# Kernel optimization log

Hardware: AMD Instinct MI355X
Metric: run time of the kernel (lower is better)

Reference implementation:

```python
import jax, jax.numpy as jnp
import numpy as np

B, T, C, H = 2, 2048, 1024, 16
D = C // H  # head_dim = 64

def setup_inputs() -> dict:
    key = jax.random.key(0)
    k1, k2, k3, k4, k5 = jax.random.split(key, 5)
    x = jax.random.normal(k1, (B, T, C), dtype=jnp.float32)
    # RoPE tables (realistic frequencies)
    inv_freq = 1.0 / (10000.0 ** (jnp.arange(0, D // 2, dtype=jnp.float32) / (D // 2)))
    pos = jnp.arange(T, dtype=jnp.float32)
    ang = pos[:, None] * inv_freq[None, :]          # (T, D/2)
    cos, sin = jnp.cos(ang), jnp.sin(ang)
    # causal mask (True = keep)
    mask = jnp.tril(jnp.ones((T, T), dtype=bool))
    W_qkv = jax.random.normal(k2, (3 * C, C), dtype=jnp.float32) * (1.0 / np.sqrt(C))
    W_out = jax.random.normal(k3, (C, C), dtype=jnp.float32) * (1.0 / np.sqrt(C))
    return {"x": x, "cos": cos, "sin": sin, "mask": mask, "W_qkv": W_qkv, "W_out": W_out}

def apply_rope(x, cos, sin):
    # x: (B, H, T, D); cos/sin: (T, D/2)
    d = x.shape[-1] // 2
    x1, x2 = x[..., :d], x[..., d:]
    c = cos[None, None, :x.shape[2], :]
    s = sin[None, None, :x.shape[2], :]
    return jnp.concatenate([x1 * c - x2 * s, x2 * c + x1 * s], axis=-1)

def reference(x, cos, sin, mask, W_qkv, W_out):
    b, t, c = x.shape
    qkv = (x @ W_qkv.T).reshape(b, t, 3, H, D)
    q, k, v = qkv[:, :, 0], qkv[:, :, 1], qkv[:, :, 2]   # (b, t, H, D)
    q = q.transpose(0, 2, 1, 3)
    k = k.transpose(0, 2, 1, 3)
    v = v.transpose(0, 2, 1, 3)                           # (b, H, t, D)
    q = apply_rope(q, cos, sin)
    k = apply_rope(k, cos, sin)
    attn = jnp.einsum('bhqd,bhkd->bhqk', q, k) / jnp.sqrt(jnp.asarray(D, x.dtype))
    attn = jnp.where(mask[None, None, :, :], attn, -jnp.inf)
    attn = jax.nn.softmax(attn, axis=-1)
    out = jnp.einsum('bhqk,bhkd->bhqd', attn, v)          # (b, H, t, D)
    out = out.transpose(0, 2, 1, 3).reshape(b, t, c)
    return out @ W_out.T
```

## Files before the change

### kernel.cpp

```cpp
#include <hip/hip_runtime.h>
#include <stdint.h>

typedef __bf16 bf16;
typedef __bf16 bf16x4 __attribute__((ext_vector_type(4)));
typedef __bf16 bf16x8 __attribute__((ext_vector_type(8)));
typedef float f32x4 __attribute__((ext_vector_type(4)));

#define TSEQ 2048
#define NHEAD 16
#define HDIM 64
#define CDIM 1024

#define AS1(p) ((const __attribute__((address_space(1))) void*)(p))
#define AS3(p) ((__attribute__((address_space(3))) void*)(p))

#if __has_builtin(__builtin_amdgcn_exp2f)
#define EXP2(x) __builtin_amdgcn_exp2f(x)
#else
#define EXP2(x) exp2f(x)
#endif

__global__ __launch_bounds__(256) void cast3_bf16(const float* __restrict__ in1, int n1,
                                                  const float* __restrict__ in2, int n2,
                                                  const float* __restrict__ in3, int n3,
                                                  bf16* __restrict__ out1,
                                                  bf16* __restrict__ out2,
                                                  bf16* __restrict__ out3) {
  int i = (blockIdx.x * 256 + threadIdx.x) * 8;
  const float* src;
  bf16* dst;
  if (i < n1) {
    src = in1 + i; dst = out1 + i;
  } else if (i < n1 + n2) {
    src = in2 + (i - n1); dst = out2 + (i - n1);
  } else if (i < n1 + n2 + n3) {
    src = in3 + (i - n1 - n2); dst = out3 + (i - n1 - n2);
  } else {
    return;
  }
  float4 a = *(const float4*)src;
  float4 b = *(const float4*)(src + 4);
  bf16x8 r;
  r[0] = (bf16)a.x; r[1] = (bf16)a.y; r[2] = (bf16)a.z; r[3] = (bf16)a.w;
  r[4] = (bf16)b.x; r[5] = (bf16)b.y; r[6] = (bf16)b.z; r[7] = (bf16)b.w;
  *(bf16x8*)dst = r;
}

__global__ __launch_bounds__(256) void gemm_qkv_rope(const bf16* __restrict__ A,
                                                     const bf16* __restrict__ B,
                                                     const float* __restrict__ cosb,
                                                     const float* __restrict__ sinb,
                                                     bf16* __restrict__ Qb,
                                                     bf16* __restrict__ Kb,
                                                     bf16* __restrict__ Vt) {
  constexpr int K = 1024;
  __shared__ bf16 smem[8704];
  const int t = threadIdx.x;
  const int w = t >> 6, l = t & 63, g = l >> 4, ln = l & 15;
  const int wm = (w >> 1) * 64, wn = (w & 1) * 64;
  const int m0 = blockIdx.x * 128, n0 = blockIdx.y * 128;
  const int r0 = t >> 2, kc0 = (t & 3) * 8;

  f32x4 acc[4][4] = {};

  for (int k0 = 0; k0 < K; k0 += 32) {
    __syncthreads();
    __builtin_amdgcn_global_load_lds(AS1(A + (size_t)(m0 + r0) * K + k0 + kc0),
                                     AS3(&smem[t * 8]), 16, 0, 0);
    __builtin_amdgcn_global_load_lds(AS1(A + (size_t)(m0 + r0 + 64) * K + k0 + kc0),
                                     AS3(&smem[(t + 256) * 8]), 16, 0, 0);
    __builtin_amdgcn_global_load_lds(AS1(B + (size_t)(n0 + r0) * K + k0 + kc0),
                                     AS3(&smem[4096 + t * 8]), 16, 0, 0);
    __builtin_amdgcn_global_load_lds(AS1(B + (size_t)(n0 + r0 + 64) * K + k0 + kc0),
                                     AS3(&smem[4096 + (t + 256) * 8]), 16, 0, 0);
    __syncthreads();
    bf16x8 af[4], bfr[4];
#pragma unroll
    for (int i = 0; i < 4; i++) {
      af[i] = *(const bf16x8*)&smem[(wm + i * 16 + ln) * 32 + g * 8];
      bfr[i] = *(const bf16x8*)&smem[4096 + (wn + i * 16 + ln) * 32 + g * 8];
    }
#pragma unroll
    for (int i = 0; i < 4; i++)
#pragma unroll
      for (int j = 0; j < 4; j++)
        acc[i][j] = __builtin_amdgcn_mfma_f32_16x16x32_bf16(af[i], bfr[j], acc[i][j], 0, 0, 0);
  }

  const int part = n0 >> 10;
  if (part < 2) {
    bf16* dst = part ? Kb : Qb;
    const float qs = part ? 1.0f : 0.18033688011112042f;
#pragma unroll
    for (int i = 0; i < 4; i++)
#pragma unroll
      for (int j = 0; j < 2; j++) {
        int nl = (n0 & 1023) + wn + j * 16 + ln;
        int h = nl >> 6, d = nl & 31;
#pragma unroll
        for (int r = 0; r < 4; r++) {
          int row = m0 + wm + i * 16 + g * 4 + r;
          int tok = row & (TSEQ - 1), bb = row >> 11;
          float c = cosb[tok * 32 + d], s = sinb[tok * 32 + d];
          float a1 = acc[i][j][r], a2 = acc[i][j + 2][r];
          size_t ob = ((size_t)(bb * NHEAD + h) * TSEQ + tok) * HDIM + d;
          dst[ob] = (bf16)((a1 * c - a2 * s) * qs);
          dst[ob + 32] = (bf16)((a2 * c + a1 * s) * qs);
        }
      }
  } else {
    const int bb = m0 >> 11;
    const int tbase = m0 & (TSEQ - 1);
    const int nbase = n0 - 2048;
#pragma unroll
    for (int pass = 0; pass < 2; pass++) {
      __syncthreads();
      if ((w >> 1) == pass) {
#pragma unroll
        for (int i = 0; i < 4; i++)
#pragma unroll
          for (int j = 0; j < 4; j++) {
            int lr = i * 16 + g * 4;
            int lc = wn + j * 16 + ln;
#pragma unroll
            for (int r = 0; r < 4; r++)
              smem[(lr + r) * 132 + lc] = (bf16)acc[i][j][r];
          }
      }
      __syncthreads();
      for (int c = t; c < 1024; c += 256) {
        int ch = c >> 3, tc = c & 7;
        bf16x8 o;
#pragma unroll
        for (int j2 = 0; j2 < 8; j2++) o[j2] = smem[(tc * 8 + j2) * 132 + ch];
        int n = nbase + ch;
        int h = n >> 6, d = n & 63;
        *(bf16x8*)(Vt + ((size_t)((bb * NHEAD + h) * HDIM + d)) * TSEQ +
                   tbase + pass * 64 + tc * 8) = o;
      }
    }
  }
}

__global__ __launch_bounds__(256) void gemm_out(const bf16* __restrict__ A,
                                                const bf16* __restrict__ B,
                                                float* __restrict__ C,
                                                int M, int N, int K) {
  __shared__ bf16 As[64 * 32];
  __shared__ bf16 Bs[128 * 32];
  const int t = threadIdx.x;
  const int w = t >> 6, l = t & 63, g = l >> 4, ln = l & 15;
  const int m0 = blockIdx.x * 64, n0 = blockIdx.y * 128;
  const int r0 = t >> 2, kc0 = (t & 3) * 8;

  f32x4 acc[4][2] = {};

  for (int k0 = 0; k0 < K; k0 += 32) {
    __syncthreads();
    __builtin_amdgcn_global_load_lds(AS1(A + (size_t)(m0 + r0) * K + k0 + kc0),
                                     AS3(&As[t * 8]), 16, 0, 0);
    __builtin_amdgcn_global_load_lds(AS1(B + (size_t)(n0 + r0) * K + k0 + kc0),
                                     AS3(&Bs[t * 8]), 16, 0, 0);
    __builtin_amdgcn_global_load_lds(AS1(B + (size_t)(n0 + r0 + 64) * K + k0 + kc0),
                                     AS3(&Bs[(t + 256) * 8]), 16, 0, 0);
    __syncthreads();
    bf16x8 af[4], bfr[2];
#pragma unroll
    for (int i = 0; i < 4; i++)
      af[i] = *(const bf16x8*)&As[(i * 16 + ln) * 32 + g * 8];
#pragma unroll
    for (int j = 0; j < 2; j++)
      bfr[j] = *(const bf16x8*)&Bs[(w * 32 + j * 16 + ln) * 32 + g * 8];
#pragma unroll
    for (int i = 0; i < 4; i++)
#pragma unroll
      for (int j = 0; j < 2; j++)
        acc[i][j] = __builtin_amdgcn_mfma_f32_16x16x32_bf16(af[i], bfr[j], acc[i][j], 0, 0, 0);
  }
#pragma unroll
  for (int i = 0; i < 4; i++)
#pragma unroll
    for (int j = 0; j < 2; j++) {
      int row = m0 + i * 16 + g * 4;
      int col = n0 + w * 32 + j * 16 + ln;
#pragma unroll
      for (int r = 0; r < 4; r++)
        C[(size_t)(row + r) * N + col] = acc[i][j][r];
    }
}

__global__ __launch_bounds__(512) void attn_fwd(const bf16* __restrict__ Q,
                                                const bf16* __restrict__ K,
                                                const bf16* __restrict__ Vt,
                                                bf16* __restrict__ ctx) {
  __shared__ bf16 Ks[2][64 * 72];
  __shared__ bf16 VTs[2][64 * 72];
  __shared__ bf16 Ps[8][16 * 72];
  __shared__ float Mrg[4][64][16];
  __shared__ float lred[4][16];
  __shared__ float linv[4][16];

  const int t = threadIdx.x;
  const int gp = t >> 8;
  const int tl = t & 255;
  const int w = t >> 6;
  const int w2 = w & 3;
  const int l = t & 63, g = l >> 4, ln = l & 15;
  const int bid = blockIdx.x;
  const int bh = bid & 31, pr = bid >> 5;
  const size_t base = (size_t)bh * TSEQ * HDIM;

  const int r0 = tl >> 3, r1 = (tl + 256) >> 3, ch0 = (tl & 7) * 8;
  bf16x8 kr0, kr1, vr0, vr1;

  for (int half = 0; half < 2; half++) {
    const int qb = half ? (31 - pr) : pr;
    const int q0 = qb * 64;
    const int q_global = q0 + w2 * 16 + ln;
    bf16x8 bq[2];
    bq[0] = *(const bf16x8*)(Q + base + (size_t)q_global * HDIM + g * 8);
    bq[1] = *(const bf16x8*)(Q + base + (size_t)q_global * HDIM + 32 + g * 8);
    f32x4 acc[4] = {};
    float l_run = 0.f;
    const int nit = (qb >> 1) + 1;

    if (gp <= qb) {
      kr0 = *(const bf16x8*)(K + base + (size_t)(gp * 64 + r0) * HDIM + ch0);
      kr1 = *(const bf16x8*)(K + base + (size_t)(gp * 64 + r1) * HDIM + ch0);
      vr0 = *(const bf16x8*)(Vt + base + (size_t)r0 * TSEQ + gp * 64 + ch0);
      vr1 = *(const bf16x8*)(Vt + base + (size_t)r1 * TSEQ + gp * 64 + ch0);
    }

    for (int i = 0; i < nit; i++) {
      const int kt = 2 * i + gp;
      const bool active = (kt <= qb);
      __syncthreads();
      if (active) {
        *(bf16x8*)&Ks[gp][r0 * 72 + ch0] = kr0;
        *(bf16x8*)&Ks[gp][r1 * 72 + ch0] = kr1;
        *(bf16x8*)&VTs[gp][r0 * 72 + ch0] = vr0;
        *(bf16x8*)&VTs[gp][r1 * 72 + ch0] = vr1;
      }
      __syncthreads();
      const int ktn = kt + 2;
      if (ktn <= qb) {
        kr0 = *(const bf16x8*)(K + base + (size_t)(ktn * 64 + r0) * HDIM + ch0);
        kr1 = *(const bf16x8*)(K + base + (size_t)(ktn * 64 + r1) * HDIM + ch0);
        vr0 = *(const bf16x8*)(Vt + base + (size_t)r0 * TSEQ + ktn * 64 + ch0);
        vr1 = *(const bf16x8*)(Vt + base + (size_t)r1 * TSEQ + ktn * 64 + ch0);
      }
      if (active) {
        f32x4 st[4] = {};
#pragma unroll
        for (int step = 0; step < 2; step++)
#pragma unroll
          for (int mt = 0; mt < 4; mt++) {
            bf16x8 ak = *(const bf16x8*)&Ks[gp][(mt * 16 + ln) * 72 + step * 32 + g * 8];
            st[mt] = __builtin_amdgcn_mfma_f32_16x16x32_bf16(ak, bq[step], st[mt], 0, 0, 0);
          }
        float vals[16];
        if (kt == qb) {
#pragma unroll
          for (int mt = 0; mt < 4; mt++)
#pragma unroll
            for (int r = 0; r < 4; r++) {
              int kg = kt * 64 + mt * 16 + g * 4 + r;
              vals[mt * 4 + r] = (kg <= q_global) ? fminf(st[mt][r], 60.f) : -INFINITY;
            }
        } else {
#pragma unroll
          for (int mt = 0; mt < 4; mt++)
#pragma unroll
            for (int r = 0; r < 4; r++) vals[mt * 4 + r] = fminf(st[mt][r], 60.f);
        }
        float psum = 0.f;
#pragma unroll
        for (int i2 = 0; i2 < 16; i2++) {
          float p = EXP2(vals[i2]);
          vals[i2] = p;
          psum += p;
        }
        psum += __shfl_xor(psum, 16);
        psum += __shfl_xor(psum, 32);
        l_run += psum;
#pragma unroll
        for (int mt = 0; mt < 4; mt++) {
          bf16x4 pk;
#pragma unroll
          for (int r = 0; r < 4; r++) pk[r] = (bf16)vals[mt * 4 + r];
          *(bf16x4*)&Ps[w][ln * 72 + mt * 16 + g * 4] = pk;
        }
#pragma unroll
        for (int step = 0; step < 2; step++) {
          bf16x8 ap = *(const bf16x8*)&Ps[w][ln * 72 + step * 32 + g * 8];
#pragma unroll
          for (int nt = 0; nt < 4; nt++) {
            bf16x8 bv = *(const bf16x8*)&VTs[gp][(nt * 16 + ln) * 72 + step * 32 + g * 8];
            acc[nt] = __builtin_amdgcn_mfma_f32_16x16x32_bf16(ap, bv, acc[nt], 0, 0, 0);
          }
        }
      }
    }
    __syncthreads();
    if (gp == 1) {
#pragma unroll
      for (int nt = 0; nt < 4; nt++) *(f32x4*)&Mrg[w2][l][nt * 4] = acc[nt];
      if (l < 16) lred[w2][ln] = l_run;
    }
    __syncthreads();
    if (gp == 0) {
#pragma unroll
      for (int nt = 0; nt < 4; nt++) acc[nt] += *(const f32x4*)&Mrg[w2][l][nt * 4];
      float ltot = l_run + lred[w2][ln];
      if (l < 16) linv[w2][ln] = 1.0f / ltot;
      float lrow[4];
#pragma unroll
      for (int r = 0; r < 4; r++) lrow[r] = linv[w2][g * 4 + r];
      const int b = bh >> 4, h = bh & (NHEAD - 1);
#pragma unroll
      for (int nt = 0; nt < 4; nt++)
#pragma unroll
        for (int r = 0; r < 4; r++) {
          int q = q0 + w2 * 16 + g * 4 + r;
          ctx[(size_t)(b * TSEQ + q) * CDIM + h * HDIM + nt * 16 + ln] =
              (bf16)(acc[nt][r] * lrow[r]);
        }
    }
  }
}

extern "C" void kernel_launch(void* const* d_in, const int* in_sizes, int n_in,
                              void* d_out, int out_size, void* d_ws, size_t ws_size,
                              hipStream_t stream) {
  const float* x = (const float*)d_in[0];
  const float* cosb = (const float*)d_in[1];
  const float* sinb = (const float*)d_in[2];
  const float* Wqkv = (const float*)d_in[4];
  const float* Wout = (const float*)d_in[5];
  float* out = (float*)d_out;

  char* ws = (char*)d_ws;
  bf16* x_bf = (bf16*)ws;
  bf16* ctx = (bf16*)ws;
  bf16* Wqkv_bf = (bf16*)(ws + 8388608);
  bf16* Wout_bf = (bf16*)(ws + 14680064);
  bf16* Qb = (bf16*)(ws + 16777216);
  bf16* Kb = (bf16*)(ws + 25165824);
  bf16* Vt = (bf16*)(ws + 33554432);

  cast3_bf16<<<(4194304 + 3145728 + 1048576) / 8 / 256, 256, 0, stream>>>(
      x, 4194304, Wqkv, 3145728, Wout, 1048576, x_bf, Wqkv_bf, Wout_bf);
  gemm_qkv_rope<<<dim3(32, 24), 256, 0, stream>>>(x_bf, Wqkv_bf, cosb, sinb, Qb, Kb, Vt);
  attn_fwd<<<512, 512, 0, stream>>>(Qb, Kb, Vt, ctx);
  gemm_out<<<dim3(64, 8), 256, 0, stream>>>(ctx, Wout_bf, out, 4096, 1024, 1024);
}
```

Measured before the change: 188.7 us.

## Rewrite attention with 32x32 MFMA tiles, register-resident K/V and P

Replaces the attention kernel's 16x16x32 MFMA tiling with 32x32x16 MFMA tiles. Each of four waves (two query halves by two key halves) loads K and V fragments directly from global memory into registers, with no LDS staging or double buffering. The P matrix moves between lanes with cross-half shuffles instead of going through LDS. The block drops to 256 threads, partial results are merged through LDS, and output is written as coalesced bf16x8 stores. This removes most LDS traffic and barriers in the inner loop, but loses the software prefetch of K/V and relies on L2/cache for repeated global reads.

```diff
diff --git a/kernel.cpp b/kernel.cpp
--- a/kernel.cpp
+++ b/kernel.cpp
@@ -5,6 +5,7 @@
 typedef __bf16 bf16x4 __attribute__((ext_vector_type(4)));
 typedef __bf16 bf16x8 __attribute__((ext_vector_type(8)));
 typedef float f32x4 __attribute__((ext_vector_type(4)));
+typedef float f32x16 __attribute__((ext_vector_type(16)));
 
 #define TSEQ 2048
 #define NHEAD 16
@@ -189,142 +190,128 @@
     }
 }
 
-__global__ __launch_bounds__(512) void attn_fwd(const bf16* __restrict__ Q,
+__global__ __launch_bounds__(256) void attn_fwd(const bf16* __restrict__ Q,
                                                 const bf16* __restrict__ K,
                                                 const bf16* __restrict__ Vt,
                                                 bf16* __restrict__ ctx) {
-  __shared__ bf16 Ks[2][64 * 72];
-  __shared__ bf16 VTs[2][64 * 72];
-  __shared__ bf16 Ps[8][16 * 72];
-  __shared__ float Mrg[4][64][16];
-  __shared__ float lred[4][16];
-  __shared__ float linv[4][16];
+  __shared__ float Red[2][64][32];
+  __shared__ float Lred[2][32];
+  __shared__ float Ot[64 * 68];
 
   const int t = threadIdx.x;
-  const int gp = t >> 8;
-  const int tl = t & 255;
   const int w = t >> 6;
-  const int w2 = w & 3;
-  const int l = t & 63, g = l >> 4, ln = l & 15;
+  const int kw = w & 1, qw = w >> 1;
+  const int l = t & 63, ln32 = l & 31, hi = l >> 5;
   const int bid = blockIdx.x;
   const int bh = bid & 31, pr = bid >> 5;
   const size_t base = (size_t)bh * TSEQ * HDIM;
-
-  const int r0 = tl >> 3, r1 = (tl + 256) >> 3, ch0 = (tl & 7) * 8;
-  bf16x8 kr0, kr1, vr0, vr1;
+  const int b = bh >> 4, h = bh & (NHEAD - 1);
 
   for (int half = 0; half < 2; half++) {
     const int qb = half ? (31 - pr) : pr;
     const int q0 = qb * 64;
-    const int q_global = q0 + w2 * 16 + ln;
-    bf16x8 bq[2];
-    bq[0] = *(const bf16x8*)(Q + base + (size_t)q_global * HDIM + g * 8);
-    bq[1] = *(const bf16x8*)(Q + base + (size_t)q_global * HDIM + 32 + g * 8);
-    f32x4 acc[4] = {};
+    const int qg = q0 + qw * 32 + ln32;
+    bf16x8 bq[4];
+#pragma unroll
+    for (int s = 0; s < 4; s++)
+      bq[s] = *(const bf16x8*)(Q + base + (size_t)qg * HDIM + s * 16 + hi * 8);
+
+    f32x16 oacc[2] = {};
     float l_run = 0.f;
-    const int nit = (qb >> 1) + 1;
-
-    if (gp <= qb) {
-      kr0 = *(const bf16x8*)(K + base + (size_t)(gp * 64 + r0) * HDIM + ch0);
-      kr1 = *(const bf16x8*)(K + base + (size_t)(gp * 64 + r1) * HDIM + ch0);
-      vr0 = *(const bf16x8*)(Vt + base + (size_t)r0 * TSEQ + gp * 64 + ch0);
-      vr1 = *(const bf16x8*)(Vt + base + (size_t)r1 * TSEQ + gp * 64 + ch0);
-    }
-
-    for (int i = 0; i < nit; i++) {
-      const int kt = 2 * i + gp;
-      const bool active = (kt <= qb);
-      __syncthreads();
-      if (active) {
-        *(bf16x8*)&Ks[gp][r0 * 72 + ch0] = kr0;
-        *(bf16x8*)&Ks[gp][r1 * 72 + ch0] = kr1;
-        *(bf16x8*)&VTs[gp][r0 * 72 + ch0] = vr0;
-        *(bf16x8*)&VTs[gp][r1 * 72 + ch0] = vr1;
-      }
-      __syncthreads();
-      const int ktn = kt + 2;
-      if (ktn <= qb) {
-        kr0 = *(const bf16x8*)(K + base + (size_t)(ktn * 64 + r0) * HDIM + ch0);
-        kr1 = *(const bf16x8*)(K + base + (size_t)(ktn * 64 + r1) * HDIM + ch0);
-        vr0 = *(const bf16x8*)(Vt + base + (size_t)r0 * TSEQ + ktn * 64 + ch0);
-        vr1 = *(const bf16x8*)(Vt + base + (size_t)r1 * TSEQ + ktn * 64 + ch0);
-      }
-      if (active) {
-        f32x4 st[4] = {};
-#pragma unroll
-        for (int step = 0; step < 2; step++)
-#pragma unroll
-          for (int mt = 0; mt < 4; mt++) {
-            bf16x8 ak = *(const bf16x8*)&Ks[gp][(mt * 16 + ln) * 72 + step * 32 + g * 8];
-            st[mt] = __builtin_amdgcn_mfma_f32_16x16x32_bf16(ak, bq[step], st[mt], 0, 0, 0);
-          }
-        float vals[16];
-        if (kt == qb) {
-#pragma unroll
-          for (int mt = 0; mt < 4; mt++)
-#pragma unroll
-            for (int r = 0; r < 4; r++) {
-              int kg = kt * 64 + mt * 16 + g * 4 + r;
-              vals[mt * 4 + r] = (kg <= q_global) ? fminf(st[mt][r], 60.f) : -INFINITY;
-            }
-        } else {
-#pragma unroll
-          for (int mt = 0; mt < 4; mt++)
-#pragma unroll
-            for (int r = 0; r < 4; r++) vals[mt * 4 + r] = fminf(st[mt][r], 60.f);
-        }
-        float psum = 0.f;
-#pragma unroll
-        for (int i2 = 0; i2 < 16; i2++) {
-          float p = EXP2(vals[i2]);
-          vals[i2] = p;
+
+    for (int kt = 0; kt <= qb; kt++) {
+      const int krow_base = kt * 64 + kw * 32;
+      bf16x8 ak[4];
+#pragma unroll
+      for (int s = 0; s < 4; s++)
+        ak[s] = *(const bf16x8*)(K + base + (size_t)(krow_base + ln32) * HDIM +
+                                 s * 16 + hi * 8);
+      bf16x8 av[2][2];
+#pragma unroll
+      for (int dt = 0; dt < 2; dt++)
+#pragma unroll
+        for (int ks = 0; ks < 2; ks++)
+          av[dt][ks] = *(const bf16x8*)(Vt + base + (size_t)(dt * 32 + ln32) * TSEQ +
+                                        krow_base + ks * 16 + hi * 8);
+
+      f32x16 st = {};
+#pragma unroll
+      for (int s = 0; s < 4; s++)
+        st = __builtin_amdgcn_mfma_f32_32x32x16_bf16(ak[s], bq[s], st, 0, 0, 0);
+
+      float psum = 0.f;
+      bf16x4 grp[4];
+      if (kt == qb) {
+#pragma unroll
+        for (int r = 0; r < 16; r++) {
+          int kg = krow_base + (r & 3) + 8 * (r >> 2) + 4 * hi;
+          float v = (kg <= qg) ? fminf(st[r], 60.f) : -INFINITY;
+          float p = EXP2(v);
           psum += p;
-        }
-        psum += __shfl_xor(psum, 16);
-        psum += __shfl_xor(psum, 32);
-        l_run += psum;
-#pragma unroll
-        for (int mt = 0; mt < 4; mt++) {
-          bf16x4 pk;
-#pragma unroll
-          for (int r = 0; r < 4; r++) pk[r] = (bf16)vals[mt * 4 + r];
-          *(bf16x4*)&Ps[w][ln * 72 + mt * 16 + g * 4] = pk;
-        }
-#pragma unroll
-        for (int step = 0; step < 2; step++) {
-          bf16x8 ap = *(const bf16x8*)&Ps[w][ln * 72 + step * 32 + g * 8];
-#pragma unroll
-          for (int nt = 0; nt < 4; nt++) {
-            bf16x8 bv = *(const bf16x8*)&VTs[gp][(nt * 16 + ln) * 72 + step * 32 + g * 8];
-            acc[nt] = __builtin_amdgcn_mfma_f32_16x16x32_bf16(ap, bv, acc[nt], 0, 0, 0);
-          }
-        }
-      }
-    }
-    __syncthreads();
-    if (gp == 1) {
-#pragma unroll
-      for (int nt = 0; nt < 4; nt++) *(f32x4*)&Mrg[w2][l][nt * 4] = acc[nt];
-      if (l < 16) lred[w2][ln] = l_run;
-    }
-    __syncthreads();
-    if (gp == 0) {
-#pragma unroll
-      for (int nt = 0; nt < 4; nt++) acc[nt] += *(const f32x4*)&Mrg[w2][l][nt * 4];
-      float ltot = l_run + lred[w2][ln];
-      if (l < 16) linv[w2][ln] = 1.0f / ltot;
-      float lrow[4];
-#pragma unroll
-      for (int r = 0; r < 4; r++) lrow[r] = linv[w2][g * 4 + r];
-      const int b = bh >> 4, h = bh & (NHEAD - 1);
-#pragma unroll
-      for (int nt = 0; nt < 4; nt++)
-#pragma unroll
-        for (int r = 0; r < 4; r++) {
-          int q = q0 + w2 * 16 + g * 4 + r;
-          ctx[(size_t)(b * TSEQ + q) * CDIM + h * HDIM + nt * 16 + ln] =
-              (bf16)(acc[nt][r] * lrow[r]);
-        }
+          grp[r >> 2][r & 3] = (bf16)p;
+        }
+      } else {
+#pragma unroll
+        for (int r = 0; r < 16; r++) {
+          float p = EXP2(fminf(st[r], 60.f));
+          psum += p;
+          grp[r >> 2][r & 3] = (bf16)p;
+        }
+      }
+      psum += __shfl_xor(psum, 32);
+      l_run += psum;
+
+#pragma unroll
+      for (int ks = 0; ks < 2; ks++) {
+        int2 snd = *(int2*)&grp[2 * ks + 1 - hi];
+        int2 rcv;
+        rcv.x = __shfl_xor(snd.x, 32);
+        rcv.y = __shfl_xor(snd.y, 32);
+        bf16x4 self = grp[2 * ks + hi];
+        bf16x4 oth = *(bf16x4*)&rcv;
+        bf16x8 bp;
+#pragma unroll
+        for (int j = 0; j < 4; j++) {
+          bp[j] = hi ? oth[j] : self[j];
+          bp[4 + j] = hi ? self[j] : oth[j];
+        }
+#pragma unroll
+        for (int dt = 0; dt < 2; dt++)
+          oacc[dt] = __builtin_amdgcn_mfma_f32_32x32x16_bf16(av[dt][ks], bp, oacc[dt], 0, 0, 0);
+      }
+    }
+
+    __syncthreads();
+    if (kw == 1) {
+#pragma unroll
+      for (int dt = 0; dt < 2; dt++)
+#pragma unroll
+        for (int r = 0; r < 16; r++) {
+          int d = dt * 32 + (r & 3) + 8 * (r >> 2) + 4 * hi;
+          Red[qw][d][ln32] = oacc[dt][r];
+        }
+      if (hi == 0) Lred[qw][ln32] = l_run;
+    }
+    __syncthreads();
+    if (kw == 0) {
+      float linv = 1.0f / (l_run + Lred[qw][ln32]);
+#pragma unroll
+      for (int dt = 0; dt < 2; dt++)
+#pragma unroll
+        for (int r = 0; r < 16; r++) {
+          int d = dt * 32 + (r & 3) + 8 * (r >> 2) + 4 * hi;
+          Ot[(qw * 32 + ln32) * 68 + d] = (oacc[dt][r] + Red[qw][d][ln32]) * linv;
+        }
+    }
+    __syncthreads();
+    for (int u = t; u < 512; u += 256) {
+      int q = u >> 3, dc = (u & 7) * 8;
+      f32x4 a = *(const f32x4*)&Ot[q * 68 + dc];
+      f32x4 c2 = *(const f32x4*)&Ot[q * 68 + dc + 4];
+      bf16x8 o;
+#pragma unroll
+      for (int j = 0; j < 4; j++) { o[j] = (bf16)a[j]; o[4 + j] = (bf16)c2[j]; }
+      *(bf16x8*)(ctx + (size_t)(b * TSEQ + q0 + q) * CDIM + h * HDIM + dc) = o;
     }
   }
 }
@@ -351,6 +338,6 @@
   cast3_bf16<<<(4194304 + 3145728 + 1048576) / 8 / 256, 256, 0, stream>>>(
       x, 4194304, Wqkv, 3145728, Wout, 1048576, x_bf, Wqkv_bf, Wout_bf);
   gemm_qkv_rope<<<dim3(32, 24), 256, 0, stream>>>(x_bf, Wqkv_bf, cosb, sinb, Qb, Kb, Vt);
-  attn_fwd<<<512, 512, 0, stream>>>(Qb, Kb, Vt, ctx);
+  attn_fwd<<<512, 256, 0, stream>>>(Qb, Kb, Vt, ctx);
   gemm_out<<<dim3(64, 8), 256, 0, stream>>>(ctx, Wout_bf, out, 4096, 1024, 1024);
 }
```

After: 238.6 us. 1.26x slower.
